# Kernel optimization log

Measured on AMD Instinct MI355X. Metric: run time of the kernel, lower is better.

Reference implementation:

```python
import jax, jax.numpy as jnp
import numpy as np

N_NODES = 100000
N_EDGES = 3200000
N_GRAPHS = 64
IN_DIM, HID_DIM, EMB_DIM = 4, 64, 32


def setup_inputs() -> dict:
    key = jax.random.key(0)
    ks = jax.random.split(key, 9)
    x = jax.random.normal(ks[0], (N_NODES, IN_DIM), dtype=jnp.float32)
    edge_index = jax.random.randint(ks[1], (2, N_EDGES), 0, N_NODES, dtype=jnp.int32)
    batch = jnp.sort(jax.random.randint(ks[2], (N_NODES,), 0, N_GRAPHS, dtype=jnp.int32))
    def glorot(k, fan_in, fan_out):
        s = jnp.sqrt(6.0 / (fan_in + fan_out))
        return jax.random.uniform(k, (fan_in, fan_out), jnp.float32, -s, s)
    return {
        "x": x,
        "W1": glorot(ks[3], IN_DIM, HID_DIM), "b1": jnp.zeros((HID_DIM,), jnp.float32),
        "W2": glorot(ks[4], HID_DIM, HID_DIM), "b2": jnp.zeros((HID_DIM,), jnp.float32),
        "W3": glorot(ks[5], HID_DIM, EMB_DIM), "b3": jnp.zeros((EMB_DIM,), jnp.float32),
        "edge_index": edge_index,
        "batch": batch,
    }


def _gcn_conv(x, W, b, src, dst, dis):
    # PyG GCNConv: h = x W; out_i = sum_{j->i} (d_i d_j)^{-1/2} h_j  (self-loops included) + b
    h = x @ W                                   # [N, F_out]
    norm = dis[src] * dis[dst]                  # [E]
    agg = jax.ops.segment_sum(norm[:, None] * h[src], dst, num_segments=N_NODES)
    agg = agg + (dis * dis)[:, None] * h        # self-loop contribution (norm = d_i^{-1})
    return agg + b


def reference(x, W1, b1, W2, b2, W3, b3, edge_index, batch):
    src, dst = edge_index[0], edge_index[1]
    # degree with self-loops (counts in-edges at dst, matching PyG default flow)
    deg = jax.ops.segment_sum(jnp.ones_like(dst, dtype=jnp.float32), dst,
                              num_segments=N_NODES) + 1.0
    dis = jax.lax.rsqrt(deg)                    # deg_inv_sqrt, deg >= 1 always

    h = jax.nn.relu(_gcn_conv(x, W1, b1, src, dst, dis))
    h = jax.nn.relu(_gcn_conv(h, W2, b2, src, dst, dis))
    emb = _gcn_conv(h, W3, b3, src, dst, dis)   # [N, EMB_DIM]

    ones = jnp.ones((N_NODES,), jnp.float32)
    cnt = jax.ops.segment_sum(ones, batch, num_segments=N_GRAPHS)  # [G]
    feat_mean = jax.ops.segment_sum(emb, batch, num_segments=N_GRAPHS) / jnp.maximum(cnt, 1.0)[:, None]
    feat_max = jax.ops.segment_max(emb, batch, num_segments=N_GRAPHS)
    return jnp.concatenate([feat_mean, feat_max], axis=1)  # [G, 2*EMB_DIM]
```

## Files before the change

### kernel.cpp

```cpp
#include <hip/hip_runtime.h>
#include <hip/hip_bf16.h>

#define N_GRAPHS 64
#define TPAD 68
#define NT 16
#define TSHIFT 13


#define EBH 8192
__global__ void bucket_hist_kernel(const int* __restrict__ dst, int* __restrict__ bcnt,
                                   int E, int nbuck) {
    __shared__ int lh[512];
    const int tid = threadIdx.x;
    for (int i = tid; i < nbuck; i += 256) lh[i] = 0;
    __syncthreads();
    const int e0 = blockIdx.x * EBH;
    const int e1 = min(e0 + EBH, E);
    for (int e = e0 + tid; e < e1; e += 256)
        atomicAdd(&lh[((unsigned)dst[e]) >> 8], 1);
    __syncthreads();
    for (int i = tid; i < nbuck; i += 256) {
        int c = lh[i];
        if (c) atomicAdd(&bcnt[i], c);
    }
}

__global__ void bucket_scan_kernel(const int* __restrict__ bcnt, int* __restrict__ bbase,
                                   int* __restrict__ bcur, int nbuck) {
    __shared__ int sh[512];
    const int tid = threadIdx.x;
    int v = (tid < nbuck) ? bcnt[tid] : 0;
    sh[tid] = v;
    __syncthreads();
    for (int off = 1; off < 512; off <<= 1) {
        int t = (tid >= off) ? sh[tid - off] : 0;
        __syncthreads();
        sh[tid] += t;
        __syncthreads();
    }
    if (tid < nbuck) { int e = sh[tid] - v; bbase[tid] = e; bcur[tid] = e; }
    if (tid == nbuck - 1) bbase[nbuck] = sh[tid];
}


#define EBC 4096
__global__ void binscatter_kernel(const int* __restrict__ src, const int* __restrict__ dst,
                                  int* __restrict__ bcur, unsigned* __restrict__ binned,
                                  int E, int nbuck) {
    __shared__ int lhist[512];
    __shared__ int lbase[512];
    const int tid = threadIdx.x;
    const int e0 = blockIdx.x * EBC;
    const int e1 = min(e0 + EBC, E);
    for (int i = tid; i < nbuck; i += 256) lhist[i] = 0;
    __syncthreads();
    for (int e = e0 + tid; e < e1; e += 256) atomicAdd(&lhist[((unsigned)dst[e]) >> 8], 1);
    __syncthreads();
    for (int i = tid; i < nbuck; i += 256) {
        int c = lhist[i];
        lbase[i] = (c > 0) ? atomicAdd(&bcur[i], c) : 0;
        lhist[i] = 0;
    }
    __syncthreads();
    for (int e = e0 + tid; e < e1; e += 256) {
        int d = dst[e];
        int b = ((unsigned)d) >> 8;
        int off = atomicAdd(&lhist[b], 1);
        binned[lbase[b] + off] = ((unsigned)(d & 255) << 24) | (unsigned)src[e];
    }
}


__global__ void build_bucket_kernel(const unsigned* __restrict__ binned, const int* __restrict__ bbase,
                                    const float* __restrict__ x, int* __restrict__ rs,
                                    float* __restrict__ dis_g, float* __restrict__ Xs,
                                    int* __restrict__ col, int n) {
    __shared__ int cnt2[256 * NT];
    __shared__ int wsum[4];
    const int b = blockIdx.x;
    const int node_base = b << 8;
    const int nb = min(256, n - node_base);
    const int tid = threadIdx.x;
    #pragma unroll
    for (int t = 0; t < NT; ++t) cnt2[tid * NT + t] = 0;
    __syncthreads();
    const int e0 = bbase[b], e1 = bbase[b + 1];
    for (int e = e0 + tid; e < e1; e += 256) {
        unsigned v = binned[e];
        int dloc = v >> 24;
        int t = (int)((v & 0xFFFFFFu) >> TSHIFT);
        atomicAdd(&cnt2[dloc * NT + t], 1);
    }
    __syncthreads();
    int deg = 0;
    #pragma unroll
    for (int t = 0; t < NT; ++t) deg += cnt2[tid * NT + t];
    const int lane = tid & 63, wid = tid >> 6;
    int s = deg;
    #pragma unroll
    for (int off = 1; off < 64; off <<= 1) {
        int t = __shfl_up(s, off);
        if (lane >= off) s += t;
    }
    if (lane == 63) wsum[wid] = s;
    __syncthreads();
    int woff = 0;
    for (int w = 0; w < wid; ++w) woff += wsum[w];
    const int excl = woff + s - deg;
    int run = e0 + excl;
    #pragma unroll
    for (int t = 0; t < NT; ++t) {
        int c = cnt2[tid * NT + t];
        cnt2[tid * NT + t] = run;
        run += c;
    }
    if (tid < nb) {
        int node = node_base + tid;
        rs[node] = e0 + excl;
        float d = rsqrtf((float)deg + 1.0f);
        dis_g[node] = d;
        float4 xv = *(const float4*)&x[node * 4];
        *(float4*)&Xs[node * 4] = make_float4(d * xv.x, d * xv.y, d * xv.z, d * xv.w);
    }
    if (tid == 0 && node_base + nb == n) rs[n] = e1;
    __syncthreads();
    for (int e = e0 + tid; e < e1; e += 256) {
        unsigned v = binned[e];
        int dloc = v >> 24;
        int srcv = (int)(v & 0xFFFFFFu);
        int t = srcv >> TSHIFT;
        int p = atomicAdd(&cnt2[dloc * NT + t], 1);
        col[p] = srcv;
    }
}


__global__ void agg4_kernel(const float* __restrict__ Xs, const int* __restrict__ col,
                            const int* __restrict__ rs, const float* __restrict__ dis,
                            float* __restrict__ aggX, int n) {
    int i = blockIdx.x * blockDim.x + threadIdx.x;
    if (i >= n) return;
    int e = rs[i];
    const int end = rs[i + 1];
    float4 a0 = make_float4(0, 0, 0, 0), a1 = make_float4(0, 0, 0, 0);
    for (; e + 2 <= end; e += 2) {
        int s0 = col[e], s1 = col[e + 1];
        float4 v0 = *(const float4*)&Xs[s0 * 4];
        float4 v1 = *(const float4*)&Xs[s1 * 4];
        a0.x += v0.x; a0.y += v0.y; a0.z += v0.z; a0.w += v0.w;
        a1.x += v1.x; a1.y += v1.y; a1.z += v1.z; a1.w += v1.w;
    }
    if (e < end) {
        float4 v = *(const float4*)&Xs[col[e] * 4];
        a0.x += v.x; a0.y += v.y; a0.z += v.z; a0.w += v.w;
    }
    float4 self = *(const float4*)&Xs[i * 4];
    float d = dis[i];
    float4 r = make_float4(d * (a0.x + a1.x + self.x), d * (a0.y + a1.y + self.y),
                           d * (a0.z + a1.z + self.z), d * (a0.w + a1.w + self.w));
    *(float4*)&aggX[i * 4] = r;
}


__global__ void fused_l1_kernel(const float* __restrict__ aggX, const float* __restrict__ W1,
                                const float* __restrict__ b1, const float* __restrict__ W2,
                                const float* __restrict__ dis, float* __restrict__ t, int n) {
    __shared__ float W1s[256];
    __shared__ float b1s[64];
    __shared__ float Wt[64 * TPAD];
    __shared__ float Hs[64 * TPAD];
    const int tid = threadIdx.x;
    const int base = blockIdx.x * 64;
    if (tid < 256) W1s[tid] = W1[tid];
    if (tid < 64) b1s[tid] = b1[tid];
    for (int idx = tid; idx < 4096; idx += 256) {
        int k = idx >> 6, f = idx & 63;
        Wt[f * TPAD + k] = W2[idx];
    }
    __syncthreads();
    for (int idx = tid; idx < 4096; idx += 256) {
        int nn = idx >> 6, k = idx & 63;
        int node = base + nn;
        float v = 0.0f;
        if (node < n) {
            float4 a = *(const float4*)&aggX[node * 4];
            v = fmaxf(a.x * W1s[k] + a.y * W1s[64 + k] + a.z * W1s[128 + k] + a.w * W1s[192 + k]
                      + b1s[k], 0.0f);
        }
        Hs[nn * TPAD + k] = v;
    }
    __syncthreads();
    const int tf = tid & 15;
    const int tn = tid >> 4;
    float acc[4][4] = {};
    for (int k = 0; k < 64; k += 4) {
        float4 w4[4], h4[4];
        #pragma unroll
        for (int ff = 0; ff < 4; ++ff) w4[ff] = *(const float4*)&Wt[(tf * 4 + ff) * TPAD + k];
        #pragma unroll
        for (int nn = 0; nn < 4; ++nn) h4[nn] = *(const float4*)&Hs[(tn * 4 + nn) * TPAD + k];
        #pragma unroll
        for (int nn = 0; nn < 4; ++nn)
            #pragma unroll
            for (int ff = 0; ff < 4; ++ff)
                acc[nn][ff] += h4[nn].x * w4[ff].x + h4[nn].y * w4[ff].y +
                               h4[nn].z * w4[ff].z + h4[nn].w * w4[ff].w;
    }
    #pragma unroll
    for (int nn = 0; nn < 4; ++nn) {
        int node = base + tn * 4 + nn;
        if (node < n) {
            float d = dis[node];
            float4 o = make_float4(d * acc[nn][0], d * acc[nn][1], d * acc[nn][2], d * acc[nn][3]);
            *(float4*)&t[node * 64 + tf * 4] = o;
        }
    }
}


__global__ void agg64_fused_kernel(const float* __restrict__ t, const int* __restrict__ col,
                                   const int* __restrict__ rs, const float* __restrict__ dis,
                                   const float* __restrict__ b2, const float* __restrict__ W3,
                                   float* __restrict__ t32, int n) {
    __shared__ float W3s[2048];
    __shared__ float rrow[4 * 65];
    __shared__ float disl[4];
    const int tid = threadIdx.x;
    for (int idx = tid; idx < 2048; idx += 256) W3s[idx] = W3[idx];
    const int w = tid >> 6, f = tid & 63;
    const int i = blockIdx.x * 4 + w;
    if (i < n) {
        float acc0 = 0.0f, acc1 = 0.0f;
        int e = rs[i];
        const int end = rs[i + 1];
        for (; e + 8 <= end; e += 8) {
            int s0 = col[e],     s1 = col[e + 1], s2 = col[e + 2], s3 = col[e + 3];
            int s4 = col[e + 4], s5 = col[e + 5], s6 = col[e + 6], s7 = col[e + 7];
            float v0 = t[s0 * 64 + f], v1 = t[s1 * 64 + f], v2 = t[s2 * 64 + f], v3 = t[s3 * 64 + f];
            float v4 = t[s4 * 64 + f], v5 = t[s5 * 64 + f], v6 = t[s6 * 64 + f], v7 = t[s7 * 64 + f];
            acc0 += v0; acc1 += v1; acc0 += v2; acc1 += v3;
            acc0 += v4; acc1 += v5; acc0 += v6; acc1 += v7;
        }
        for (; e < end; ++e) acc0 += t[col[e] * 64 + f];
        float di = dis[i];
        float r = fmaxf(di * (acc0 + acc1 + t[i * 64 + f]) + b2[f], 0.0f);
        rrow[w * 65 + f] = r;
        if (f == 0) disl[w] = di;
    }
    __syncthreads();
    if (tid < 128) {
        int q = tid >> 5, c = tid & 31;
        int node = blockIdx.x * 4 + q;
        if (node < n) {
            float dot = 0.0f;
            #pragma unroll
            for (int ff = 0; ff < 64; ++ff)
                dot += rrow[q * 65 + ff] * W3s[ff * 32 + c];
            t32[node * 32 + c] = disl[q] * dot;
        }
    }
}


__global__ void agg32_kernel(const float* __restrict__ t, const int* __restrict__ col,
                             const int* __restrict__ rs, const float* __restrict__ dis,
                             const float* __restrict__ b, float* __restrict__ out, int n) {
    int gid = blockIdx.x * blockDim.x + threadIdx.x;
    int i = gid >> 5, f = threadIdx.x & 31;
    if (i >= n) return;
    float acc0 = 0.0f, acc1 = 0.0f;
    int e = rs[i];
    const int end = rs[i + 1];
    for (; e + 8 <= end; e += 8) {
        int s0 = col[e],     s1 = col[e + 1], s2 = col[e + 2], s3 = col[e + 3];
        int s4 = col[e + 4], s5 = col[e + 5], s6 = col[e + 6], s7 = col[e + 7];
        float v0 = t[s0 * 32 + f], v1 = t[s1 * 32 + f], v2 = t[s2 * 32 + f], v3 = t[s3 * 32 + f];
        float v4 = t[s4 * 32 + f], v5 = t[s5 * 32 + f], v6 = t[s6 * 32 + f], v7 = t[s7 * 32 + f];
        acc0 += v0; acc1 += v1; acc0 += v2; acc1 += v3;
        acc0 += v4; acc1 += v5; acc0 += v6; acc1 += v7;
    }
    for (; e < end; ++e) acc0 += t[col[e] * 32 + f];
    out[i * 32 + f] = dis[i] * (acc0 + acc1 + t[i * 32 + f]) + b[f];
}


__device__ __forceinline__ unsigned mapf(float v) {
    unsigned u = __float_as_uint(v);
    return u ^ ((u & 0x80000000u) ? 0xFFFFFFFFu : 0x80000000u);
}

#define MAPPED_NEG_INF 0x007FFFFFu

__global__ void init_readout_kernel(float* __restrict__ gsum, unsigned* __restrict__ gmax,
                                    int* __restrict__ gcnt) {
    int idx = blockIdx.x * blockDim.x + threadIdx.x;
    if (idx < N_GRAPHS * 32) { gsum[idx] = 0.0f; gmax[idx] = MAPPED_NEG_INF; }
    if (idx < N_GRAPHS) gcnt[idx] = 0;
}

#define R_CHUNK 512
__global__ void readout_kernel(const float* __restrict__ emb, const int* __restrict__ batch,
                               float* __restrict__ gsum, unsigned* __restrict__ gmax,
                               int* __restrict__ gcnt, int n) {
    __shared__ float ssum[N_GRAPHS * 32];
    __shared__ unsigned smax[N_GRAPHS * 32];
    __shared__ int scnt[N_GRAPHS];
    const int tid = threadIdx.x;
    for (int idx = tid; idx < N_GRAPHS * 32; idx += 256) { ssum[idx] = 0.0f; smax[idx] = MAPPED_NEG_INF; }
    if (tid < N_GRAPHS) scnt[tid] = 0;
    __syncthreads();
    const int lane = tid & 31, grp = tid >> 5;
    const int start = blockIdx.x * R_CHUNK;
    const int end = min(start + R_CHUNK, n);
    for (int i = start + grp; i < end; i += 8) {
        int g = batch[i];
        float v = emb[i * 32 + lane];
        atomicAdd(&ssum[g * 32 + lane], v);
        atomicMax(&smax[g * 32 + lane], mapf(v));
        if (lane == 0) atomicAdd(&scnt[g], 1);
    }
    __syncthreads();
    for (int idx = tid; idx < N_GRAPHS * 32; idx += 256) {
        int g = idx >> 5;
        if (scnt[g] > 0) {
            atomicAdd(&gsum[idx], ssum[idx]);
            atomicMax(&gmax[idx], smax[idx]);
        }
    }
    if (tid < N_GRAPHS && scnt[tid] > 0) atomicAdd(&gcnt[tid], scnt[tid]);
}

__global__ void finalize_kernel(const float* __restrict__ gsum, const unsigned* __restrict__ gmax,
                                const int* __restrict__ gcnt, float* __restrict__ out) {
    int idx = blockIdx.x * blockDim.x + threadIdx.x;
    if (idx >= N_GRAPHS * 32) return;
    int g = idx >> 5, f = idx & 31;
    float c = fmaxf((float)gcnt[g], 1.0f);
    out[g * 64 + f] = gsum[idx] / c;
    unsigned u = gmax[idx];
    unsigned bits = (u & 0x80000000u) ? (u ^ 0x80000000u) : ~u;
    out[g * 64 + 32 + f] = __uint_as_float(bits);
}


extern "C" void kernel_launch(void* const* d_in, const int* in_sizes, int n_in,
                              void* d_out, int out_size, void* d_ws, size_t ws_size,
                              hipStream_t stream) {
    const float* x  = (const float*)d_in[0];
    const float* W1 = (const float*)d_in[1];
    const float* b1 = (const float*)d_in[2];
    const float* W2 = (const float*)d_in[3];
    const float* b2 = (const float*)d_in[4];
    const float* W3 = (const float*)d_in[5];
    const float* b3 = (const float*)d_in[6];
    const int* edge_index = (const int*)d_in[7];
    const int* batch = (const int*)d_in[8];
    float* out = (float*)d_out;

    const int N = in_sizes[0] / 4;
    const int E = in_sizes[7] / 2;
    const int* src = edge_index;
    const int* dst = edge_index + E;
    const int nbuck = (N + 255) >> 8;

    char* p = (char*)d_ws;
    auto alloc = [&](size_t bytes) { void* r = (void*)p; p += (bytes + 255) & ~(size_t)255; return r; };
    int*      rs   = (int*)alloc((size_t)(N + 1) * 4);
    float*    dis  = (float*)alloc((size_t)N * 4);
    int*      col  = (int*)alloc((size_t)E * 4);
    float*    Xs   = (float*)alloc((size_t)N * 4 * 4);
    float*    aggX = (float*)alloc((size_t)N * 4 * 4);
    float*    T    = (float*)alloc((size_t)N * 64 * 4);
    float*    T32  = (float*)alloc((size_t)N * 32 * 4);
    int*      bcnt = (int*)alloc((size_t)512 * 4);
    int*      bbase= (int*)alloc((size_t)513 * 4);
    int*      bcur = (int*)alloc((size_t)512 * 4);
    float*    gsum = (float*)alloc((size_t)N_GRAPHS * 32 * 4);
    unsigned* gmax = (unsigned*)alloc((size_t)N_GRAPHS * 32 * 4);
    int*      gcnt = (int*)alloc((size_t)N_GRAPHS * 4);
    unsigned* binned = (unsigned*)T;
    float*    H32    = T;
    (void)ws_size; (void)n_in; (void)out_size;

    const int gN = (N + 255) / 256;

    hipMemsetAsync(bcnt, 0, 512 * 4, stream);
    bucket_hist_kernel<<<(E + EBH - 1) / EBH, 256, 0, stream>>>(dst, bcnt, E, nbuck);
    bucket_scan_kernel<<<1, 512, 0, stream>>>(bcnt, bbase, bcur, nbuck);
    binscatter_kernel<<<(E + EBC - 1) / EBC, 256, 0, stream>>>(src, dst, bcur, binned, E, nbuck);
    build_bucket_kernel<<<nbuck, 256, 0, stream>>>(binned, bbase, x, rs, dis, Xs, col, N);

    agg4_kernel<<<gN, 256, 0, stream>>>(Xs, col, rs, dis, aggX, N);
    fused_l1_kernel<<<(N + 63) / 64, 256, 0, stream>>>(aggX, W1, b1, W2, dis, T, N);
    agg64_fused_kernel<<<(N + 3) / 4, 256, 0, stream>>>(T, col, rs, dis, b2, W3, T32, N);
    agg32_kernel<<<(N * 32 + 255) / 256, 256, 0, stream>>>(T32, col, rs, dis, b3, H32, N);

    init_readout_kernel<<<(N_GRAPHS * 32 + 255) / 256, 256, 0, stream>>>(gsum, gmax, gcnt);
    readout_kernel<<<(N + R_CHUNK - 1) / R_CHUNK, 256, 0, stream>>>(H32, batch, gsum, gmax, gcnt, N);
    finalize_kernel<<<(N_GRAPHS * 32 + 255) / 256, 256, 0, stream>>>(gsum, gmax, gcnt, out);
}
```

Measured before the change: 378.5 us.

## Tile neighbor gathers by source-node range across multi-node persistent waves

Replaces the per-node aggregation kernels for the 64- and 32-wide layers with a templated kernel in which each wavefront handles many destination nodes. It sweeps source-index tiles (NT ranges of 2^TSHIFT nodes) in lockstep, so the concurrent gathers hit a bounded slice of the feature table and reuse cache better. This relies on col being sorted by source within each row. The cost is serialized per-edge loads with data-dependent break loops, more divergence, and block-wide syncs inside the fused W3 projection.

```diff
diff --git a/kernel.cpp b/kernel.cpp
--- a/kernel.cpp
+++ b/kernel.cpp
@@ -218,69 +218,83 @@
 }
 
 
-__global__ void agg64_fused_kernel(const float* __restrict__ t, const int* __restrict__ col,
-                                   const int* __restrict__ rs, const float* __restrict__ dis,
-                                   const float* __restrict__ b2, const float* __restrict__ W3,
-                                   float* __restrict__ t32, int n) {
+template <int F, int NPW, bool FUSE_W3>
+__global__ __launch_bounds__(256, 4)
+void agg_tiled_kernel(const float* __restrict__ t, const int* __restrict__ col,
+                      const int* __restrict__ rs, const float* __restrict__ dis,
+                      const float* __restrict__ bias, const float* __restrict__ W3,
+                      float* __restrict__ out, int n) {
     __shared__ float W3s[2048];
-    __shared__ float rrow[4 * 65];
-    __shared__ float disl[4];
-    const int tid = threadIdx.x;
-    for (int idx = tid; idx < 2048; idx += 256) W3s[idx] = W3[idx];
-    const int w = tid >> 6, f = tid & 63;
-    const int i = blockIdx.x * 4 + w;
-    if (i < n) {
-        float acc0 = 0.0f, acc1 = 0.0f;
-        int e = rs[i];
-        const int end = rs[i + 1];
-        for (; e + 8 <= end; e += 8) {
-            int s0 = col[e],     s1 = col[e + 1], s2 = col[e + 2], s3 = col[e + 3];
-            int s4 = col[e + 4], s5 = col[e + 5], s6 = col[e + 6], s7 = col[e + 7];
-            float v0 = t[s0 * 64 + f], v1 = t[s1 * 64 + f], v2 = t[s2 * 64 + f], v3 = t[s3 * 64 + f];
-            float v4 = t[s4 * 64 + f], v5 = t[s5 * 64 + f], v6 = t[s6 * 64 + f], v7 = t[s7 * 64 + f];
-            acc0 += v0; acc1 += v1; acc0 += v2; acc1 += v3;
-            acc0 += v4; acc1 += v5; acc0 += v6; acc1 += v7;
-        }
-        for (; e < end; ++e) acc0 += t[col[e] * 64 + f];
-        float di = dis[i];
-        float r = fmaxf(di * (acc0 + acc1 + t[i * 64 + f]) + b2[f], 0.0f);
-        rrow[w * 65 + f] = r;
-        if (f == 0) disl[w] = di;
-    }
-    __syncthreads();
-    if (tid < 128) {
-        int q = tid >> 5, c = tid & 31;
-        int node = blockIdx.x * 4 + q;
-        if (node < n) {
-            float dot = 0.0f;
-            #pragma unroll
-            for (int ff = 0; ff < 64; ++ff)
-                dot += rrow[q * 65 + ff] * W3s[ff * 32 + c];
-            t32[node * 32 + c] = disl[q] * dot;
-        }
-    }
-}
-
-
-__global__ void agg32_kernel(const float* __restrict__ t, const int* __restrict__ col,
-                             const int* __restrict__ rs, const float* __restrict__ dis,
-                             const float* __restrict__ b, float* __restrict__ out, int n) {
-    int gid = blockIdx.x * blockDim.x + threadIdx.x;
-    int i = gid >> 5, f = threadIdx.x & 31;
-    if (i >= n) return;
-    float acc0 = 0.0f, acc1 = 0.0f;
-    int e = rs[i];
-    const int end = rs[i + 1];
-    for (; e + 8 <= end; e += 8) {
-        int s0 = col[e],     s1 = col[e + 1], s2 = col[e + 2], s3 = col[e + 3];
-        int s4 = col[e + 4], s5 = col[e + 5], s6 = col[e + 6], s7 = col[e + 7];
-        float v0 = t[s0 * 32 + f], v1 = t[s1 * 32 + f], v2 = t[s2 * 32 + f], v3 = t[s3 * 32 + f];
-        float v4 = t[s4 * 32 + f], v5 = t[s5 * 32 + f], v6 = t[s6 * 32 + f], v7 = t[s7 * 32 + f];
-        acc0 += v0; acc1 += v1; acc0 += v2; acc1 += v3;
-        acc0 += v4; acc1 += v5; acc0 += v6; acc1 += v7;
-    }
-    for (; e < end; ++e) acc0 += t[col[e] * 32 + f];
-    out[i * 32 + f] = dis[i] * (acc0 + acc1 + t[i * 32 + f]) + b[f];
+    __shared__ float rowbuf[4][2][64];
+    const int tid = threadIdx.x;
+    if (FUSE_W3) {
+        for (int idx = tid; idx < 2048; idx += 256) W3s[idx] = W3[idx];
+        __syncthreads();
+    }
+    const int lane = tid & 63;
+    const int w = tid >> 6;
+    const int gw = blockIdx.x * 4 + w;
+    const int h = (F == 64) ? 0 : (lane >> 5);
+    const int f = lane & (F - 1);
+    const int npn = 64 / F;
+    const int base = gw * NPW * npn;
+
+    int cur[NPW], endr[NPW];
+    float acc[NPW];
+    #pragma unroll
+    for (int k = 0; k < NPW; ++k) {
+        int i = base + k * npn + h;
+        bool valid = (i < n);
+        cur[k] = valid ? rs[i] : 0;
+        endr[k] = valid ? rs[i + 1] : 0;
+        acc[k] = 0.0f;
+    }
+
+    for (int tp = 0; tp < NT; ++tp) {
+        #pragma unroll
+        for (int k = 0; k < NPW; ++k) {
+            int e = cur[k];
+            const int en = endr[k];
+            while (e < en) {
+                int s = col[e];
+                if ((s >> TSHIFT) != tp) break;
+                acc[k] += t[s * F + f];
+                ++e;
+            }
+            cur[k] = e;
+        }
+    }
+
+    if (FUSE_W3) {
+        const int hh = lane >> 5, c = lane & 31;
+        #pragma unroll
+        for (int k = 0; k < NPW; k += 2) {
+            const int i0 = base + k;
+            const int i1 = base + k + 1;
+            float d0 = 0.0f, d1 = 0.0f;
+            float r0 = 0.0f, r1 = 0.0f;
+            if (i0 < n) { d0 = dis[i0]; r0 = fmaxf(d0 * (acc[k] + t[i0 * 64 + f]) + bias[f], 0.0f); }
+            if (k + 1 < NPW && i1 < n) { d1 = dis[i1]; r1 = fmaxf(d1 * (acc[k + 1] + t[i1 * 64 + f]) + bias[f], 0.0f); }
+            rowbuf[w][0][lane] = r0;
+            rowbuf[w][1][lane] = r1;
+            __syncthreads();
+            const int ii = (hh == 0) ? i0 : i1;
+            const bool wr = (hh == 0) ? (i0 < n) : (k + 1 < NPW && i1 < n);
+            if (wr) {
+                float dot = 0.0f;
+                #pragma unroll
+                for (int ff = 0; ff < 64; ++ff) dot += rowbuf[w][hh][ff] * W3s[ff * 32 + c];
+                out[ii * 32 + c] = ((hh == 0) ? d0 : d1) * dot;
+            }
+            __syncthreads();
+        }
+    } else {
+        #pragma unroll
+        for (int k = 0; k < NPW; ++k) {
+            int i = base + k * npn + h;
+            if (i < n) out[i * F + f] = dis[i] * (acc[k] + t[i * F + f]) + bias[f];
+        }
+    }
 }
 
 
@@ -392,8 +406,8 @@
 
     agg4_kernel<<<gN, 256, 0, stream>>>(Xs, col, rs, dis, aggX, N);
     fused_l1_kernel<<<(N + 63) / 64, 256, 0, stream>>>(aggX, W1, b1, W2, dis, T, N);
-    agg64_fused_kernel<<<(N + 3) / 4, 256, 0, stream>>>(T, col, rs, dis, b2, W3, T32, N);
-    agg32_kernel<<<(N * 32 + 255) / 256, 256, 0, stream>>>(T32, col, rs, dis, b3, H32, N);
+    agg_tiled_kernel<64, 25, true><<<1024, 256, 0, stream>>>(T, col, rs, dis, b2, W3, T32, N);
+    agg_tiled_kernel<32, 13, false><<<1024, 256, 0, stream>>>(T32, col, rs, dis, b3, W3, H32, N);
 
     init_readout_kernel<<<(N_GRAPHS * 32 + 255) / 256, 256, 0, stream>>>(gsum, gmax, gcnt);
     readout_kernel<<<(N + R_CHUNK - 1) / R_CHUNK, 256, 0, stream>>>(H32, batch, gsum, gmax, gcnt, N);
```

Measured after the change: 1.144 ms. 3.02x slower.
